# Kernel optimization log

Hardware: AMD Instinct MI355X
Metric: run time of the kernel (lower is better)

## Reference

```python
import jax, jax.numpy as jnp
import numpy as np

N_NODES = 50000
N_EDGES = 800000
NUM_GRAPHS = 4
IN_DIM, HID_DIM, OUT_DIM = 1024, 128, 1
MAX_RISK = 5.0


def gcn_conv(x, W, b, src, dst, n):
    """PyG GCNConv: add self-loops, sym-normalize, gather-GEMM-scatter."""
    loop = jnp.arange(n, dtype=src.dtype)
    s = jnp.concatenate([src, loop])
    d = jnp.concatenate([dst, loop])
    deg = jax.ops.segment_sum(jnp.ones_like(d, dtype=x.dtype), d, num_segments=n)
    dinv = jnp.where(deg > 0, jax.lax.rsqrt(deg), 0.0)
    norm = dinv[s] * dinv[d]  # [E+N]
    xw = x @ W                # dense GEMM first (fewer FLOPs than per-edge)
    msg = xw[s] * norm[:, None]          # irregular gather, [E+N, out]
    out = jax.ops.segment_sum(msg, d, num_segments=n)  # scatter-add
    return out + b


def setup_inputs() -> dict:
    key = jax.random.key(0)
    ks = jax.random.split(key, 12)
    x = jax.random.normal(ks[0], (N_NODES, IN_DIM), dtype=jnp.float32)
    edge_index = jax.random.randint(ks[1], (2, N_EDGES), 0, N_NODES, dtype=jnp.int64)
    batch = jnp.sort(jax.random.randint(ks[2], (N_NODES,), 0, NUM_GRAPHS, dtype=jnp.int64))

    def glorot(k, fan_in, fan_out):
        s = np.sqrt(6.0 / (fan_in + fan_out)).astype(np.float32)
        return jax.random.uniform(k, (fan_in, fan_out), jnp.float32, -s, s)

    params = {
        'W0': glorot(ks[3], IN_DIM, HID_DIM),  'b0': jnp.zeros((HID_DIM,), jnp.float32),
        'W1': glorot(ks[4], HID_DIM, HID_DIM), 'b1': jnp.zeros((HID_DIM,), jnp.float32),
        'W2': glorot(ks[5], HID_DIM, HID_DIM), 'b2': jnp.zeros((HID_DIM,), jnp.float32),
        'Wl1': glorot(ks[6], 2 * HID_DIM, HID_DIM), 'bl1': jnp.zeros((HID_DIM,), jnp.float32),
        'Wl2': glorot(ks[7], HID_DIM, HID_DIM // 2), 'bl2': jnp.zeros((HID_DIM // 2,), jnp.float32),
        'Wl3': glorot(ks[8], HID_DIM // 2, OUT_DIM), 'bl3': jnp.zeros((OUT_DIM,), jnp.float32),
    }
    return dict(x=x, edge_index=edge_index, batch=batch, **params)


def reference(x, edge_index, batch, W0, b0, W1, b1, W2, b2, Wl1, bl1, Wl2, bl2, Wl3, bl3):
    n = x.shape[0]
    src, dst = edge_index[0], edge_index[1]
    h = jax.nn.relu(gcn_conv(x, W0, b0, src, dst, n))
    h = jax.nn.relu(gcn_conv(h, W1, b1, src, dst, n))
    h = jax.nn.relu(gcn_conv(h, W2, b2, src, dst, n))
    # global max pool + global mean pool per graph
    gmax = jax.ops.segment_max(h, batch, num_segments=NUM_GRAPHS)
    gsum = jax.ops.segment_sum(h, batch, num_segments=NUM_GRAPHS)
    cnt = jax.ops.segment_sum(jnp.ones((n,), h.dtype), batch, num_segments=NUM_GRAPHS)
    gmean = gsum / jnp.maximum(cnt, 1.0)[:, None]
    g = jnp.concatenate([gmax, gmean], axis=1)  # [G, 2*hid]
    g = jax.nn.relu(g @ Wl1 + bl1)
    g = jax.nn.relu(g @ Wl2 + bl2)
    out = g @ Wl3 + bl3
    return jnp.minimum(out, MAX_RISK)
```

## Files before the change

kernel.cpp:

```cpp
#include <hip/hip_runtime.h>
#include <math.h>

#define HID 128
#define NGRAPH 4

typedef int idx_t;
typedef short bf16x8 __attribute__((ext_vector_type(8)));
typedef float f32x4 __attribute__((ext_vector_type(4)));
typedef _Float16 f16x8 __attribute__((ext_vector_type(8)));

__device__ inline ushort f2bf(float f) {
  uint u = __float_as_uint(f);
  u += 0x7FFF + ((u >> 16) & 1);
  return (ushort)(u >> 16);
}
__device__ inline float bf2f(ushort h) { return __uint_as_float(((uint)h) << 16); }

__device__ inline int sw(int row, int slot) {
  return (row << 5) + ((slot ^ ((row >> 1) & 3)) << 3);
}

__global__ __launch_bounds__(256) void k_count(const idx_t* __restrict__ dst,
                                               int* __restrict__ cnt, int E) {
  int e = blockIdx.x * 256 + threadIdx.x;
  if (e < E) atomicAdd(&cnt[dst[e]], 1);
}

#define SC 1024
__global__ __launch_bounds__(256) void k_scan1(const int* __restrict__ cnt,
                                               int* __restrict__ bsum, int n) {
  __shared__ int sh[256];
  int base = blockIdx.x * SC + threadIdx.x * 4;
  int s = 0;
#pragma unroll
  for (int j = 0; j < 4; ++j) { int i = base + j; if (i < n) s += cnt[i]; }
  sh[threadIdx.x] = s;
  __syncthreads();
  for (int o = 128; o > 0; o >>= 1) {
    if (threadIdx.x < o) sh[threadIdx.x] += sh[threadIdx.x + o];
    __syncthreads();
  }
  if (threadIdx.x == 0) bsum[blockIdx.x] = sh[0];
}

__global__ __launch_bounds__(64) void k_scan2(const int* __restrict__ bsum,
                                              int* __restrict__ boff,
                                              int* __restrict__ off, int nb, int n) {
  int lane = threadIdx.x;
  int v = (lane < nb) ? bsum[lane] : 0;
  for (int d = 1; d < 64; d <<= 1) {
    int t = __shfl_up(v, d);
    if (lane >= d) v += t;
  }
  int ex = __shfl_up(v, 1);
  if (lane == 0) ex = 0;
  if (lane < nb) boff[lane] = ex;
  if (lane == nb - 1) off[n] = v;
}

__global__ __launch_bounds__(256) void k_scan3(const int* __restrict__ cnt,
                                               const int* __restrict__ boff,
                                               int* __restrict__ off,
                                               float* __restrict__ dinv, int n) {
  __shared__ int sh[256];
  int base = blockIdx.x * SC + threadIdx.x * 4;
  int c[4];
  int s = 0;
#pragma unroll
  for (int j = 0; j < 4; ++j) {
    int i = base + j;
    c[j] = (i < n) ? cnt[i] : 0;
    s += c[j];
  }
  sh[threadIdx.x] = s;
  __syncthreads();
  for (int o = 1; o < 256; o <<= 1) {
    int t = (threadIdx.x >= (unsigned)o) ? sh[threadIdx.x - o] : 0;
    __syncthreads();
    sh[threadIdx.x] += t;
    __syncthreads();
  }
  int ex = sh[threadIdx.x] - s + boff[blockIdx.x];
#pragma unroll
  for (int j = 0; j < 4; ++j) {
    int i = base + j;
    if (i < n) {
      off[i] = ex;
      dinv[i] = 1.0f / sqrtf((float)c[j] + 1.0f);
      ex += c[j];
    }
  }
}

__global__ __launch_bounds__(256) void k_fill(const idx_t* __restrict__ src,
                                              const idx_t* __restrict__ dst,
                                              const int* __restrict__ off,
                                              const float* __restrict__ dinv,
                                              int* __restrict__ fillc,
                                              int2* __restrict__ edata, int E) {
  int e = blockIdx.x * 256 + threadIdx.x;
  if (e < E) {
    int s = src[e], d = dst[e];
    int p = atomicAdd(&fillc[d], 1);
    float w = dinv[s] * dinv[d];
    edata[off[d] + p] = make_int2(s, __float_as_int(w));
  }
}

__global__ __launch_bounds__(256) void k_wsplit(const float* __restrict__ W,
                                                ushort* __restrict__ Wh,
                                                ushort* __restrict__ Wl, int K) {
  int i = blockIdx.x * 256 + threadIdx.x;
  if (i >= K * HID) return;
  int k = i >> 7, n = i & 127;
  float f = W[i];
  ushort h = f2bf(f);
  Wh[(size_t)n * K + k] = h;
  Wl[(size_t)n * K + k] = f2bf(f - bf2f(h));
}

template <int K, int KS>
__global__ __launch_bounds__(256) void k_gemm_mfma(const float* __restrict__ X,
                                                   const ushort* __restrict__ Wh,
                                                   const ushort* __restrict__ Wl,
                                                   float* __restrict__ Ypart,
                                                   _Float16* __restrict__ Y16,
                                                   int M) {
  __shared__ __align__(16) ushort Ah[128 * 32];
  __shared__ __align__(16) ushort Al[128 * 32];
  __shared__ __align__(16) ushort Bh[128 * 32];
  __shared__ __align__(16) ushort Bl[128 * 32];
  int tid = threadIdx.x;
  int wid = tid >> 6, lane = tid & 63;
  int lrow = lane & 15, kg = lane >> 4;
  int row0 = blockIdx.x * 128;
  constexpr int KC = K / KS;
  int kbase = (KS > 1) ? blockIdx.y * KC : 0;
  f32x4 acc[2][8] = {};

  for (int k0 = kbase; k0 < kbase + KC; k0 += 32) {
#pragma unroll
    for (int p = 0; p < 2; ++p) {
      int g = tid + (p << 8);
      int r = g >> 2, s = g & 3;
      int grow = row0 + r;
      float xv[8] = {0.f, 0.f, 0.f, 0.f, 0.f, 0.f, 0.f, 0.f};
      if (grow < M) {
        const float4 v0 = *(const float4*)&X[(size_t)grow * K + k0 + s * 8];
        const float4 v1 = *(const float4*)&X[(size_t)grow * K + k0 + s * 8 + 4];
        xv[0] = v0.x; xv[1] = v0.y; xv[2] = v0.z; xv[3] = v0.w;
        xv[4] = v1.x; xv[5] = v1.y; xv[6] = v1.z; xv[7] = v1.w;
      }
      bf16x8 hv, lv;
#pragma unroll
      for (int j = 0; j < 8; ++j) {
        ushort hb = f2bf(xv[j]);
        hv[j] = (short)hb;
        lv[j] = (short)f2bf(xv[j] - bf2f(hb));
      }
      *(bf16x8*)&Ah[sw(r, s)] = hv;
      *(bf16x8*)&Al[sw(r, s)] = lv;
    }
#pragma unroll
    for (int p = 0; p < 2; ++p) {
      int g = tid + (p << 8);
      int c = g >> 2, s = g & 3;
      *(bf16x8*)&Bh[sw(c, s)] = *(const bf16x8*)&Wh[(size_t)c * K + k0 + s * 8];
      *(bf16x8*)&Bl[sw(c, s)] = *(const bf16x8*)&Wl[(size_t)c * K + k0 + s * 8];
    }
    __syncthreads();

    bf16x8 ah[2], al[2];
#pragma unroll
    for (int mi = 0; mi < 2; ++mi) {
      int r = wid * 32 + mi * 16 + lrow;
      ah[mi] = *(const bf16x8*)&Ah[sw(r, kg)];
      al[mi] = *(const bf16x8*)&Al[sw(r, kg)];
    }
#pragma unroll
    for (int ni = 0; ni < 8; ++ni) {
      int c = ni * 16 + lrow;
      bf16x8 bh = *(const bf16x8*)&Bh[sw(c, kg)];
      bf16x8 bl = *(const bf16x8*)&Bl[sw(c, kg)];
#pragma unroll
      for (int mi = 0; mi < 2; ++mi) {
        acc[mi][ni] = __builtin_amdgcn_mfma_f32_16x16x32_bf16(ah[mi], bh, acc[mi][ni], 0, 0, 0);
        acc[mi][ni] = __builtin_amdgcn_mfma_f32_16x16x32_bf16(al[mi], bh, acc[mi][ni], 0, 0, 0);
        acc[mi][ni] = __builtin_amdgcn_mfma_f32_16x16x32_bf16(ah[mi], bl, acc[mi][ni], 0, 0, 0);
      }
    }
    __syncthreads();
  }
  if (KS > 1) {
    float* yp = Ypart + (size_t)blockIdx.y * M * HID;
#pragma unroll
    for (int mi = 0; mi < 2; ++mi)
#pragma unroll
      for (int ni = 0; ni < 8; ++ni)
#pragma unroll
        for (int r = 0; r < 4; ++r) {
          int grow = row0 + wid * 32 + mi * 16 + kg * 4 + r;
          if (grow < M) yp[(size_t)grow * HID + ni * 16 + lrow] = acc[mi][ni][r];
        }
  } else {
#pragma unroll
    for (int mi = 0; mi < 2; ++mi)
#pragma unroll
      for (int ni = 0; ni < 8; ++ni)
#pragma unroll
        for (int r = 0; r < 4; ++r) {
          int grow = row0 + wid * 32 + mi * 16 + kg * 4 + r;
          if (grow < M)
            Y16[(size_t)grow * HID + ni * 16 + lrow] = (_Float16)acc[mi][ni][r];
        }
  }
}

__global__ __launch_bounds__(256) void k_red(const float* __restrict__ part,
                                             _Float16* __restrict__ o16,
                                             size_t total) {
  size_t i = ((size_t)blockIdx.x * 256 + threadIdx.x) * 4;
  if (i >= total) return;
  float4 a = *(const float4*)&part[i];
  float4 b = *(const float4*)&part[i + total];
  float4 c = *(const float4*)&part[i + 2 * total];
  float4 d = *(const float4*)&part[i + 3 * total];
  _Float16 r[4];
  r[0] = (_Float16)(a.x + b.x + c.x + d.x);
  r[1] = (_Float16)(a.y + b.y + c.y + d.y);
  r[2] = (_Float16)(a.z + b.z + c.z + d.z);
  r[3] = (_Float16)(a.w + b.w + c.w + d.w);
  *(short4*)&o16[i] = *(short4*)r;
}

__global__ __launch_bounds__(256) void k_agg16(const _Float16* __restrict__ xh,
                                               const float* __restrict__ dinv,
                                               const int* __restrict__ off,
                                               const int2* __restrict__ edata,
                                               const float* __restrict__ bias,
                                               float* __restrict__ hout, int n) {
  int v = blockIdx.x * 4 + (threadIdx.x >> 6);
  if (v >= n) return;
  int lane = threadIdx.x & 63;
  int grp = lane >> 4, gl = lane & 15;
  int fb = gl * 8;
  float acc[8] = {0.f, 0.f, 0.f, 0.f, 0.f, 0.f, 0.f, 0.f};
  int j0 = off[v], j1 = off[v + 1];
  for (int j = j0 + grp; j < j1; j += 4) {
    int2 e = edata[j];
    float w = __int_as_float(e.y);
    f16x8 m = *(const f16x8*)&xh[(size_t)e.x * HID + fb];
#pragma unroll
    for (int q = 0; q < 8; ++q) acc[q] = fmaf(w, (float)m[q], acc[q]);
  }
#pragma unroll
  for (int q = 0; q < 8; ++q) {
    acc[q] += __shfl_xor(acc[q], 16);
    acc[q] += __shfl_xor(acc[q], 32);
  }
  if (grp == 0) {
    float dv = dinv[v], dv2 = dv * dv;
    f16x8 sv = *(const f16x8*)&xh[(size_t)v * HID + fb];
    const float4 b0 = *(const float4*)&bias[fb];
    const float4 b1 = *(const float4*)&bias[fb + 4];
    float4 o0, o1;
    o0.x = fmaxf(fmaf(dv2, (float)sv[0], acc[0]) + b0.x, 0.f);
    o0.y = fmaxf(fmaf(dv2, (float)sv[1], acc[1]) + b0.y, 0.f);
    o0.z = fmaxf(fmaf(dv2, (float)sv[2], acc[2]) + b0.z, 0.f);
    o0.w = fmaxf(fmaf(dv2, (float)sv[3], acc[3]) + b0.w, 0.f);
    o1.x = fmaxf(fmaf(dv2, (float)sv[4], acc[4]) + b1.x, 0.f);
    o1.y = fmaxf(fmaf(dv2, (float)sv[5], acc[5]) + b1.y, 0.f);
    o1.z = fmaxf(fmaf(dv2, (float)sv[6], acc[6]) + b1.z, 0.f);
    o1.w = fmaxf(fmaf(dv2, (float)sv[7], acc[7]) + b1.w, 0.f);
    *(float4*)&hout[(size_t)v * HID + fb] = o0;
    *(float4*)&hout[(size_t)v * HID + fb + 4] = o1;
  }
}

__global__ __launch_bounds__(256) void k_gcnt(const idx_t* __restrict__ batch,
                                              int* __restrict__ gcnt, int n) {
  __shared__ int h[NGRAPH];
  int tid = threadIdx.x;
  if (tid < NGRAPH) h[tid] = 0;
  __syncthreads();
  int i = blockIdx.x * 256 + tid;
  if (i < n) atomicAdd(&h[batch[i]], 1);
  __syncthreads();
  if (tid < NGRAPH && h[tid]) atomicAdd(&gcnt[tid], h[tid]);
}

__global__ __launch_bounds__(128) void k_pool(const float* __restrict__ h,
                                              const idx_t* __restrict__ batch,
                                              float* __restrict__ gmax,
                                              float* __restrict__ gsum, int n) {
  int f = threadIdx.x;
  int v0 = blockIdx.x * 128;
  int cur = -1;
  float mx = 0.f, sm = 0.f;
  for (int i = 0; i < 128; ++i) {
    int v = v0 + i;
    if (v >= n) break;
    int g = batch[v];
    if (g != cur) {
      if (cur >= 0) {
        atomicMax((int*)&gmax[cur * HID + f], __float_as_int(mx));
        atomicAdd(&gsum[cur * HID + f], sm);
      }
      cur = g; mx = 0.f; sm = 0.f;
    }
    float val = h[(size_t)v * HID + f];
    mx = fmaxf(mx, val);
    sm += val;
  }
  if (cur >= 0) {
    atomicMax((int*)&gmax[cur * HID + f], __float_as_int(mx));
    atomicAdd(&gsum[cur * HID + f], sm);
  }
}

__global__ __launch_bounds__(256) void k_mlp(const float* __restrict__ gmax,
                                             const float* __restrict__ gsum,
                                             const int* __restrict__ gcnt,
                                             const float* __restrict__ Wl1,
                                             const float* __restrict__ bl1,
                                             const float* __restrict__ Wl2,
                                             const float* __restrict__ bl2,
                                             const float* __restrict__ Wl3,
                                             const float* __restrict__ bl3,
                                             float* __restrict__ out) {
  __shared__ float G[NGRAPH][2 * HID];
  __shared__ float H1[NGRAPH][HID];
  __shared__ float H2[NGRAPH][HID / 2];
  int t = threadIdx.x;
  for (int i = t; i < NGRAPH * 2 * HID; i += 256) {
    int gi = i >> 8, j = i & 255;
    float val;
    if (j < HID) val = gmax[gi * HID + j];
    else val = gsum[gi * HID + (j - HID)] / fmaxf((float)gcnt[gi], 1.0f);
    G[gi][j] = val;
  }
  __syncthreads();
  for (int i = t; i < NGRAPH * HID; i += 256) {
    int gi = i >> 7, j = i & 127;
    float a = bl1[j];
    for (int k = 0; k < 2 * HID; ++k) a = fmaf(G[gi][k], Wl1[k * HID + j], a);
    H1[gi][j] = fmaxf(a, 0.f);
  }
  __syncthreads();
  {
    int gi = t >> 6, j = t & 63;
    float a = bl2[j];
    for (int k = 0; k < HID; ++k) a = fmaf(H1[gi][k], Wl2[k * 64 + j], a);
    H2[gi][j] = fmaxf(a, 0.f);
  }
  __syncthreads();
  if (t < NGRAPH) {
    float a = bl3[0];
    for (int k = 0; k < 64; ++k) a = fmaf(H2[t][k], Wl3[k], a);
    out[t] = fminf(a, 5.0f);
  }
}

extern "C" void kernel_launch(void* const* d_in, const int* in_sizes, int n_in,
                              void* d_out, int out_size, void* d_ws, size_t ws_size,
                              hipStream_t stream) {
  const float* x   = (const float*)d_in[0];
  const idx_t* ei  = (const idx_t*)d_in[1];
  const idx_t* bat = (const idx_t*)d_in[2];
  const float* W0 = (const float*)d_in[3];  const float* b0 = (const float*)d_in[4];
  const float* W1 = (const float*)d_in[5];  const float* b1 = (const float*)d_in[6];
  const float* W2 = (const float*)d_in[7];  const float* b2 = (const float*)d_in[8];
  const float* Wl1 = (const float*)d_in[9];  const float* bl1 = (const float*)d_in[10];
  const float* Wl2 = (const float*)d_in[11]; const float* bl2 = (const float*)d_in[12];
  const float* Wl3 = (const float*)d_in[13]; const float* bl3 = (const float*)d_in[14];
  float* out = (float*)d_out;

  const int N = in_sizes[2];
  const int E = in_sizes[1] / 2;
  const idx_t* srcv = ei;
  const idx_t* dstv = ei + E;
  const int nb = (N + SC - 1) / SC;

  char* ws = (char*)d_ws;
  size_t o = 0;
  auto alloc = [&](size_t bytes) -> void* {
    void* p = ws + o;
    o = (o + bytes + 255) & ~(size_t)255;
    return p;
  };
  _Float16* xh   = (_Float16*)alloc((size_t)N * HID * 2);
  float* bufB    = (float*)alloc((size_t)N * HID * 4);
  float* part    = (float*)alloc((size_t)4 * N * HID * 4);
  float* dinv = (float*)alloc((size_t)N * 4);
  int* cnt    = (int*)alloc((size_t)N * 4);
  int* off    = (int*)alloc((size_t)(N + 1) * 4);
  int* fillc  = (int*)alloc((size_t)N * 4);
  int2* edata = (int2*)alloc((size_t)E * 8);
  int* bsum   = (int*)alloc(64 * 4);
  int* boff   = (int*)alloc(64 * 4);
  ushort* Wh0 = (ushort*)alloc((size_t)1024 * HID * 2);
  ushort* Wl0 = (ushort*)alloc((size_t)1024 * HID * 2);
  ushort* Wh1 = (ushort*)alloc((size_t)HID * HID * 2);
  ushort* Wlo1 = (ushort*)alloc((size_t)HID * HID * 2);
  ushort* Wh2 = (ushort*)alloc((size_t)HID * HID * 2);
  ushort* Wlo2 = (ushort*)alloc((size_t)HID * HID * 2);
  float* gmax = (float*)alloc(NGRAPH * HID * 4);
  float* gsum = (float*)alloc(NGRAPH * HID * 4);
  int* gcnt   = (int*)alloc(NGRAPH * 4);

  hipMemsetAsync(cnt, 0, (size_t)N * 4, stream);
  hipMemsetAsync(fillc, 0, (size_t)N * 4, stream);
  hipMemsetAsync(gmax, 0, NGRAPH * HID * 4, stream);
  hipMemsetAsync(gsum, 0, NGRAPH * HID * 4, stream);
  hipMemsetAsync(gcnt, 0, NGRAPH * 4, stream);

  k_wsplit<<<(1024 * HID + 255) / 256, 256, 0, stream>>>(W0, Wh0, Wl0, 1024);
  k_wsplit<<<(HID * HID + 255) / 256, 256, 0, stream>>>(W1, Wh1, Wlo1, HID);
  k_wsplit<<<(HID * HID + 255) / 256, 256, 0, stream>>>(W2, Wh2, Wlo2, HID);

  k_count<<<(E + 255) / 256, 256, 0, stream>>>(dstv, cnt, E);
  k_scan1<<<nb, 256, 0, stream>>>(cnt, bsum, N);
  k_scan2<<<1, 64, 0, stream>>>(bsum, boff, off, nb, N);
  k_scan3<<<nb, 256, 0, stream>>>(cnt, boff, off, dinv, N);
  k_fill<<<(E + 255) / 256, 256, 0, stream>>>(srcv, dstv, off, dinv, fillc, edata, E);

  const int gblk = (N + 127) / 128;
  const int ablk = (N + 3) / 4;
  const size_t total = (size_t)N * HID;
  k_gemm_mfma<1024, 4><<<dim3(gblk, 4), 256, 0, stream>>>(x, Wh0, Wl0, part, nullptr, N);
  k_red<<<(int)((total / 4 + 255) / 256), 256, 0, stream>>>(part, xh, total);
  k_agg16<<<ablk, 256, 0, stream>>>(xh, dinv, off, edata, b0, bufB, N);
  k_gemm_mfma<HID, 1><<<gblk, 256, 0, stream>>>(bufB, Wh1, Wlo1, nullptr, xh, N);
  k_agg16<<<ablk, 256, 0, stream>>>(xh, dinv, off, edata, b1, bufB, N);
  k_gemm_mfma<HID, 1><<<gblk, 256, 0, stream>>>(bufB, Wh2, Wlo2, nullptr, xh, N);
  k_agg16<<<ablk, 256, 0, stream>>>(xh, dinv, off, edata, b2, bufB, N);

  k_gcnt<<<(N + 255) / 256, 256, 0, stream>>>(bat, gcnt, N);
  k_pool<<<(N + 127) / 128, 128, 0, stream>>>(bufB, bat, gmax, gsum, N);
  k_mlp<<<1, 256, 0, stream>>>(gmax, gsum, gcnt, Wl1, bl1, Wl2, bl2, Wl3, bl3, out);
}
```

Before: 431.6 us.

## Rewrite GEMM with register-direct A fragments, double-buffered B, and no split-K

The GEMM kernel now loads each wave's A fragments straight from global memory into registers and converts them there, skipping the LDS staging for A. B tiles are double-buffered in LDS with register prefetch of the next K step, so global loads overlap MFMA work. The first layer drops split-K and its reduction kernel, which removes the fp32 partial-sum round trip through memory. In exchange, layer 0 launches a quarter as many blocks (about 391), which may leave CUs underused, and A loads per lane are now strided rows rather than coalesced row chunks.

```diff
diff --git a/kernel.cpp b/kernel.cpp
--- a/kernel.cpp
+++ b/kernel.cpp
@@ -8,6 +8,7 @@
 typedef short bf16x8 __attribute__((ext_vector_type(8)));
 typedef float f32x4 __attribute__((ext_vector_type(4)));
 typedef _Float16 f16x8 __attribute__((ext_vector_type(8)));
+typedef unsigned short u16x8 __attribute__((ext_vector_type(8)));
 
 __device__ inline ushort f2bf(float f) {
   uint u = __float_as_uint(f);
@@ -119,118 +120,128 @@
   Wl[(size_t)n * K + k] = f2bf(f - bf2f(h));
 }
 
-template <int K, int KS>
-__global__ __launch_bounds__(256) void k_gemm_mfma(const float* __restrict__ X,
-                                                   const ushort* __restrict__ Wh,
-                                                   const ushort* __restrict__ Wl,
-                                                   float* __restrict__ Ypart,
-                                                   _Float16* __restrict__ Y16,
-                                                   int M) {
-  __shared__ __align__(16) ushort Ah[128 * 32];
-  __shared__ __align__(16) ushort Al[128 * 32];
-  __shared__ __align__(16) ushort Bh[128 * 32];
-  __shared__ __align__(16) ushort Bl[128 * 32];
-  int tid = threadIdx.x;
-  int wid = tid >> 6, lane = tid & 63;
-  int lrow = lane & 15, kg = lane >> 4;
-  int row0 = blockIdx.x * 128;
-  constexpr int KC = K / KS;
-  int kbase = (KS > 1) ? blockIdx.y * KC : 0;
+template <int K>
+__global__ __launch_bounds__(256) void k_gemm2(const float* __restrict__ X,
+                                               const ushort* __restrict__ Wh,
+                                               const ushort* __restrict__ Wl,
+                                               _Float16* __restrict__ Y16, int M) {
+  __shared__ __align__(16) ushort BhL[2][128 * 32];
+  __shared__ __align__(16) ushort BlL[2][128 * 32];
+  const int tid = threadIdx.x;
+  const int wid = tid >> 6, lane = tid & 63;
+  const int lrow = lane & 15, kg = lane >> 4;
+  const int row0 = blockIdx.x * 128;
+  const int r0 = row0 + wid * 32 + lrow;
+  const int r1 = r0 + 16;
+  const bool ok0 = r0 < M, ok1 = r1 < M;
+  const float* xp0 = X + (size_t)(ok0 ? r0 : 0) * K + kg * 8;
+  const float* xp1 = X + (size_t)(ok1 ? r1 : 0) * K + kg * 8;
+  const int c0 = tid >> 2, s0 = tid & 3;
+  const int c1 = (tid + 256) >> 2, s1 = tid & 3;
+  const ushort* wh0 = Wh + (size_t)c0 * K + s0 * 8;
+  const ushort* wh1 = Wh + (size_t)c1 * K + s1 * 8;
+  const ushort* wl0 = Wl + (size_t)c0 * K + s0 * 8;
+  const ushort* wl1 = Wl + (size_t)c1 * K + s1 * 8;
+  const int d0 = sw(c0, s0), d1 = sw(c1, s1);
+
   f32x4 acc[2][8] = {};
-
-  for (int k0 = kbase; k0 < kbase + KC; k0 += 32) {
-#pragma unroll
-    for (int p = 0; p < 2; ++p) {
-      int g = tid + (p << 8);
-      int r = g >> 2, s = g & 3;
-      int grow = row0 + r;
-      float xv[8] = {0.f, 0.f, 0.f, 0.f, 0.f, 0.f, 0.f, 0.f};
-      if (grow < M) {
-        const float4 v0 = *(const float4*)&X[(size_t)grow * K + k0 + s * 8];
-        const float4 v1 = *(const float4*)&X[(size_t)grow * K + k0 + s * 8 + 4];
-        xv[0] = v0.x; xv[1] = v0.y; xv[2] = v0.z; xv[3] = v0.w;
-        xv[4] = v1.x; xv[5] = v1.y; xv[6] = v1.z; xv[7] = v1.w;
+  float4 aA0, aA1, aA2, aA3, aB0, aB1, aB2, aB3;
+  u16x8 bA0, bA1, bA2, bA3, bB0, bB1, bB2, bB3;
+
+#define LOAD_A(k0, a0, a1, a2, a3)                                        \
+  {                                                                       \
+    a0 = ok0 ? *(const float4*)(xp0 + (k0)) : make_float4(0, 0, 0, 0);    \
+    a1 = ok0 ? *(const float4*)(xp0 + (k0) + 4) : make_float4(0, 0, 0, 0);\
+    a2 = ok1 ? *(const float4*)(xp1 + (k0)) : make_float4(0, 0, 0, 0);    \
+    a3 = ok1 ? *(const float4*)(xp1 + (k0) + 4) : make_float4(0, 0, 0, 0);\
+  }
+#define LOAD_B(k0, b0, b1, b2, b3)                                        \
+  {                                                                       \
+    b0 = *(const u16x8*)(wh0 + (k0)); b1 = *(const u16x8*)(wh1 + (k0));   \
+    b2 = *(const u16x8*)(wl0 + (k0)); b3 = *(const u16x8*)(wl1 + (k0));   \
+  }
+#define WRITE_B(buf, b0, b1, b2, b3)                                      \
+  {                                                                       \
+    *(u16x8*)&BhL[buf][d0] = b0; *(u16x8*)&BhL[buf][d1] = b1;             \
+    *(u16x8*)&BlL[buf][d0] = b2; *(u16x8*)&BlL[buf][d1] = b3;             \
+  }
+#define CONV8(v0, v1, hdst, ldst)                                         \
+  {                                                                       \
+    float tf[8] = {v0.x, v0.y, v0.z, v0.w, v1.x, v1.y, v1.z, v1.w};       \
+    _Pragma("unroll")                                                     \
+    for (int j = 0; j < 8; ++j) {                                         \
+      ushort hb = f2bf(tf[j]);                                            \
+      hdst[j] = (short)hb;                                                \
+      ldst[j] = (short)f2bf(tf[j] - bf2f(hb));                            \
+    }                                                                     \
+  }
+#define MFMA_STEP(buf, ah0, al0, ah1, al1)                                \
+  {                                                                       \
+    _Pragma("unroll")                                                     \
+    for (int ni = 0; ni < 8; ++ni) {                                      \
+      int c = ni * 16 + lrow;                                             \
+      bf16x8 bh = *(const bf16x8*)&BhL[buf][sw(c, kg)];                   \
+      bf16x8 bl = *(const bf16x8*)&BlL[buf][sw(c, kg)];                   \
+      acc[0][ni] = __builtin_amdgcn_mfma_f32_16x16x32_bf16(ah0, bh, acc[0][ni], 0, 0, 0); \
+      acc[0][ni] = __builtin_amdgcn_mfma_f32_16x16x32_bf16(al0, bh, acc[0][ni], 0, 0, 0); \
+      acc[0][ni] = __builtin_amdgcn_mfma_f32_16x16x32_bf16(ah0, bl, acc[0][ni], 0, 0, 0); \
+      acc[1][ni] = __builtin_amdgcn_mfma_f32_16x16x32_bf16(ah1, bh, acc[1][ni], 0, 0, 0); \
+      acc[1][ni] = __builtin_amdgcn_mfma_f32_16x16x32_bf16(al1, bh, acc[1][ni], 0, 0, 0); \
+      acc[1][ni] = __builtin_amdgcn_mfma_f32_16x16x32_bf16(ah1, bl, acc[1][ni], 0, 0, 0); \
+    }                                                                     \
+  }
+
+  LOAD_A(0, aA0, aA1, aA2, aA3);
+  LOAD_B(0, bA0, bA1, bA2, bA3);
+  WRITE_B(0, bA0, bA1, bA2, bA3);
+  if (K > 32) {
+    LOAD_A(32, aB0, aB1, aB2, aB3);
+    LOAD_B(32, bB0, bB1, bB2, bB3);
+  }
+  __syncthreads();
+
+  for (int k0 = 0; k0 < K; k0 += 64) {
+    {
+      if (k0 + 32 < K) WRITE_B(1, bB0, bB1, bB2, bB3);
+      bf16x8 ah0, al0, ah1, al1;
+      CONV8(aA0, aA1, ah0, al0);
+      CONV8(aA2, aA3, ah1, al1);
+      if (k0 + 64 < K) {
+        LOAD_A(k0 + 64, aA0, aA1, aA2, aA3);
+        LOAD_B(k0 + 64, bA0, bA1, bA2, bA3);
       }
-      bf16x8 hv, lv;
-#pragma unroll
-      for (int j = 0; j < 8; ++j) {
-        ushort hb = f2bf(xv[j]);
-        hv[j] = (short)hb;
-        lv[j] = (short)f2bf(xv[j] - bf2f(hb));
+      MFMA_STEP(0, ah0, al0, ah1, al1);
+      __syncthreads();
+    }
+    if (k0 + 32 >= K) break;
+    {
+      if (k0 + 96 < K) WRITE_B(0, bA0, bA1, bA2, bA3);
+      bf16x8 ah0, al0, ah1, al1;
+      CONV8(aB0, aB1, ah0, al0);
+      CONV8(aB2, aB3, ah1, al1);
+      if (k0 + 96 < K) {
+        LOAD_A(k0 + 96, aB0, aB1, aB2, aB3);
+        LOAD_B(k0 + 96, bB0, bB1, bB2, bB3);
       }
-      *(bf16x8*)&Ah[sw(r, s)] = hv;
-      *(bf16x8*)&Al[sw(r, s)] = lv;
+      MFMA_STEP(1, ah0, al0, ah1, al1);
+      __syncthreads();
     }
-#pragma unroll
-    for (int p = 0; p < 2; ++p) {
-      int g = tid + (p << 8);
-      int c = g >> 2, s = g & 3;
-      *(bf16x8*)&Bh[sw(c, s)] = *(const bf16x8*)&Wh[(size_t)c * K + k0 + s * 8];
-      *(bf16x8*)&Bl[sw(c, s)] = *(const bf16x8*)&Wl[(size_t)c * K + k0 + s * 8];
-    }
-    __syncthreads();
-
-    bf16x8 ah[2], al[2];
-#pragma unroll
-    for (int mi = 0; mi < 2; ++mi) {
-      int r = wid * 32 + mi * 16 + lrow;
-      ah[mi] = *(const bf16x8*)&Ah[sw(r, kg)];
-      al[mi] = *(const bf16x8*)&Al[sw(r, kg)];
-    }
-#pragma unroll
-    for (int ni = 0; ni < 8; ++ni) {
-      int c = ni * 16 + lrow;
-      bf16x8 bh = *(const bf16x8*)&Bh[sw(c, kg)];
-      bf16x8 bl = *(const bf16x8*)&Bl[sw(c, kg)];
-#pragma unroll
-      for (int mi = 0; mi < 2; ++mi) {
-        acc[mi][ni] = __builtin_amdgcn_mfma_f32_16x16x32_bf16(ah[mi], bh, acc[mi][ni], 0, 0, 0);
-        acc[mi][ni] = __builtin_amdgcn_mfma_f32_16x16x32_bf16(al[mi], bh, acc[mi][ni], 0, 0, 0);
-        acc[mi][ni] = __builtin_amdgcn_mfma_f32_16x16x32_bf16(ah[mi], bl, acc[mi][ni], 0, 0, 0);
+  }
+#pragma unroll
+  for (int mi = 0; mi < 2; ++mi)
+#pragma unroll
+    for (int ni = 0; ni < 8; ++ni)
+#pragma unroll
+      for (int r = 0; r < 4; ++r) {
+        int grow = row0 + wid * 32 + mi * 16 + kg * 4 + r;
+        if (grow < M)
+          Y16[(size_t)grow * HID + ni * 16 + lrow] = (_Float16)acc[mi][ni][r];
       }
-    }
-    __syncthreads();
-  }
-  if (KS > 1) {
-    float* yp = Ypart + (size_t)blockIdx.y * M * HID;
-#pragma unroll
-    for (int mi = 0; mi < 2; ++mi)
-#pragma unroll
-      for (int ni = 0; ni < 8; ++ni)
-#pragma unroll
-        for (int r = 0; r < 4; ++r) {
-          int grow = row0 + wid * 32 + mi * 16 + kg * 4 + r;
-          if (grow < M) yp[(size_t)grow * HID + ni * 16 + lrow] = acc[mi][ni][r];
-        }
-  } else {
-#pragma unroll
-    for (int mi = 0; mi < 2; ++mi)
-#pragma unroll
-      for (int ni = 0; ni < 8; ++ni)
-#pragma unroll
-        for (int r = 0; r < 4; ++r) {
-          int grow = row0 + wid * 32 + mi * 16 + kg * 4 + r;
-          if (grow < M)
-            Y16[(size_t)grow * HID + ni * 16 + lrow] = (_Float16)acc[mi][ni][r];
-        }
-  }
-}
-
-__global__ __launch_bounds__(256) void k_red(const float* __restrict__ part,
-                                             _Float16* __restrict__ o16,
-                                             size_t total) {
-  size_t i = ((size_t)blockIdx.x * 256 + threadIdx.x) * 4;
-  if (i >= total) return;
-  float4 a = *(const float4*)&part[i];
-  float4 b = *(const float4*)&part[i + total];
-  float4 c = *(const float4*)&part[i + 2 * total];
-  float4 d = *(const float4*)&part[i + 3 * total];
-  _Float16 r[4];
-  r[0] = (_Float16)(a.x + b.x + c.x + d.x);
-  r[1] = (_Float16)(a.y + b.y + c.y + d.y);
-  r[2] = (_Float16)(a.z + b.z + c.z + d.z);
-  r[3] = (_Float16)(a.w + b.w + c.w + d.w);
-  *(short4*)&o16[i] = *(short4*)r;
+#undef LOAD_A
+#undef LOAD_B
+#undef WRITE_B
+#undef CONV8
+#undef MFMA_STEP
 }
 
 __global__ __launch_bounds__(256) void k_agg16(const _Float16* __restrict__ xh,
@@ -390,7 +401,6 @@
   };
   _Float16* xh   = (_Float16*)alloc((size_t)N * HID * 2);
   float* bufB    = (float*)alloc((size_t)N * HID * 4);
-  float* part    = (float*)alloc((size_t)4 * N * HID * 4);
   float* dinv = (float*)alloc((size_t)N * 4);
   int* cnt    = (int*)alloc((size_t)N * 4);
   int* off    = (int*)alloc((size_t)(N + 1) * 4);
@@ -426,13 +436,11 @@
 
   const int gblk = (N + 127) / 128;
   const int ablk = (N + 3) / 4;
-  const size_t total = (size_t)N * HID;
-  k_gemm_mfma<1024, 4><<<dim3(gblk, 4), 256, 0, stream>>>(x, Wh0, Wl0, part, nullptr, N);
-  k_red<<<(int)((total / 4 + 255) / 256), 256, 0, stream>>>(part, xh, total);
+  k_gemm2<1024><<<gblk, 256, 0, stream>>>(x, Wh0, Wl0, xh, N);
   k_agg16<<<ablk, 256, 0, stream>>>(xh, dinv, off, edata, b0, bufB, N);
-  k_gemm_mfma<HID, 1><<<gblk, 256, 0, stream>>>(bufB, Wh1, Wlo1, nullptr, xh, N);
+  k_gemm2<HID><<<gblk, 256, 0, stream>>>(bufB, Wh1, Wlo1, xh, N);
   k_agg16<<<ablk, 256, 0, stream>>>(xh, dinv, off, edata, b1, bufB, N);
-  k_gemm_mfma<HID, 1><<<gblk, 256, 0, stream>>>(bufB, Wh2, Wlo2, nullptr, xh, N);
+  k_gemm2<HID><<<gblk, 256, 0, stream>>>(bufB, Wh2, Wlo2, xh, N);
   k_agg16<<<ablk, 256, 0, stream>>>(xh, dinv, off, edata, b2, bufB, N);
 
   k_gcnt<<<(N + 255) / 256, 256, 0, stream>>>(bat, gcnt, N);
```

Result: faster. 391.7 us (-9.2%).
